# Optimization experiments

Measured on AMD Instinct MI355X. Metric: run time of the kernel, lower is better.

## Reference

```python
import jax, jax.numpy as jnp
import numpy as np

B = 8192
D = 128
N_CLASSES = 100
TEMPERATURE = 0.1


def setup_inputs() -> dict:
    key = jax.random.key(0)
    k1, k2 = jax.random.split(key)
    feats = jax.random.normal(k1, (B, D), dtype=jnp.float32)
    # L2-normalise as the docstring assumes
    feats = feats / jnp.linalg.norm(feats, axis=1, keepdims=True)
    labels = jax.random.randint(k2, (B,), 0, N_CLASSES, dtype=jnp.int64)
    return {"features": feats, "labels": labels}


def reference(features, labels):
    features = features.astype(jnp.float32)
    b = features.shape[0]
    sim = (features @ features.T) / TEMPERATURE            # (B, B)
    labels_eq = labels[None, :] == labels[:, None]          # (B, B)
    self_mask = ~jnp.eye(b, dtype=bool)                     # (B, B), False on diag
    pos_mask = labels_eq & self_mask

    sim_max = jax.lax.stop_gradient(jnp.max(sim, axis=1, keepdims=True))
    logits = sim - sim_max                                  # (B, B)
    exp_logits = jnp.exp(logits) * self_mask.astype(jnp.float32)
    log_sum_exp = jnp.log(jnp.sum(exp_logits, axis=1, keepdims=True) + 1e-12)
    log_prob = logits - log_sum_exp                         # (B, B)

    n_positives = jnp.sum(pos_mask.astype(jnp.float32), axis=1)  # (B,)
    valid = n_positives > 0
    mean_log_prob = jnp.sum(pos_mask.astype(jnp.float32) * log_prob, axis=1) \
        / jnp.maximum(n_positives, 1.0)

    valid_f = valid.astype(jnp.float32)
    n_valid = jnp.sum(valid_f)
    loss = -jnp.sum(mean_log_prob * valid_f) / jnp.maximum(n_valid, 1.0)
    # match torch: return 0 if no anchor has a positive
    return jnp.where(n_valid > 0, loss, jnp.float32(0.0))
```

## Files before the change

### kernel.cpp

```cpp
#include <hip/hip_runtime.h>
#include <hip/hip_bf16.h>


#define BB 8192
#define DD 128
#define NC 8
#define COLCHUNK (BB / NC)
#define ITERS (COLCHUNK / 128)
#define TEMP_INV 10.0f
#define MSHIFT 10.5f

typedef __bf16 bf16x8 __attribute__((ext_vector_type(8)));
typedef float floatx4 __attribute__((ext_vector_type(4)));

__device__ inline unsigned short f2bf(float f) {
    unsigned u = __float_as_uint(f);
    return (unsigned short)((u + 0x7FFFu + ((u >> 16) & 1u)) >> 16);
}

__global__ void supcon_detect(const unsigned short* __restrict__ feats_raw,
                              const int* __restrict__ labels_raw,
                              int* __restrict__ flags)
{
    int lane = threadIdx.x;
    unsigned ue = ((unsigned)feats_raw[2 * lane]) << 16;
    float fe = __uint_as_float(ue);
    float ve = fe * fe;
    int odd_or = labels_raw[2 * lane + 1];
#pragma unroll
    for (int m = 1; m < 64; m <<= 1) {
        ve += __shfl_xor(ve, m, 64);
        odd_or |= __shfl_xor(odd_or, m, 64);
    }
    if (lane == 0) {
        bool feats_bf16 = (ve > 0.05f) && (ve < 4.0f);
        flags[0] = feats_bf16 ? 0 : 1;
        flags[1] = (odd_or == 0) ? 1 : 0;
    }
}

__global__ __launch_bounds__(256) void supcon_convert(
    const void* __restrict__ fin, const void* __restrict__ lin,
    const int* __restrict__ flags,
    unsigned short* __restrict__ fbf, int* __restrict__ lab)
{
    int gid = blockIdx.x * 256 + threadIdx.x;
    if (flags[0]) {
        float4 v = ((const float4*)fin)[gid];
        ushort4 o;
        o.x = f2bf(v.x); o.y = f2bf(v.y); o.z = f2bf(v.z); o.w = f2bf(v.w);
        ((ushort4*)fbf)[gid] = o;
    } else {
        ((ushort4*)fbf)[gid] = ((const ushort4*)fin)[gid];
    }
    if (blockIdx.x < 32) {
        int li = blockIdx.x * 256 + threadIdx.x;
        const int* L = (const int*)lin;
        lab[li] = flags[1] ? L[2 * li] : L[li];
    }
}

__global__ __launch_bounds__(256, 2) void supcon_main(
    const unsigned short* __restrict__ Fb, const int* __restrict__ labels,
    float* __restrict__ e_part, float* __restrict__ p_part,
    float* __restrict__ n_part)
{
    __shared__ unsigned char ldsbuf[32768];
    __shared__ float red[3][128][2];

    const int tid  = threadIdx.x;
    const int lane = tid & 63;
    const int wid  = tid >> 6;
    const int wrow = wid >> 1;
    const int wcol = wid & 1;
    const int quad = lane >> 4;
    const int l16  = lane & 15;

    const int chunk   = blockIdx.x;
    const int rowbase = blockIdx.y * 128;
    const int colchunkbase = chunk * COLCHUNK;

    {
        const unsigned char* gA = (const unsigned char*)(Fb) + (size_t)rowbase * 256;
#pragma unroll
        for (int rnd = 0; rnd < 8; ++rnd) {
            int off = rnd * 4096 + tid * 16;
            int row = off >> 8;
            int g   = (off >> 4) & 15;
            int gs  = g ^ (row & 15);
            int4 v  = *(const int4*)(gA + off);
            *(int4*)(&ldsbuf[row * 256 + gs * 16]) = v;
        }
    }
    __syncthreads();

    bf16x8 afrag[4][4];
#pragma unroll
    for (int ti = 0; ti < 4; ++ti) {
        int row = wrow * 64 + ti * 16 + l16;
#pragma unroll
        for (int k = 0; k < 4; ++k) {
            int g  = k * 4 + quad;
            int gs = g ^ (row & 15);
            afrag[ti][k] = *(const bf16x8*)(&ldsbuf[row * 256 + gs * 16]);
        }
    }

    int lab_row[16];
#pragma unroll
    for (int ti = 0; ti < 4; ++ti)
#pragma unroll
        for (int r = 0; r < 4; ++r)
            lab_row[ti * 4 + r] = labels[rowbase + wrow * 64 + ti * 16 + quad * 4 + r];

    float e_acc[16], p_acc[16], n_acc[16];
#pragma unroll
    for (int i = 0; i < 16; ++i) { e_acc[i] = 0.0f; p_acc[i] = 0.0f; n_acc[i] = 0.0f; }

    __syncthreads();

    for (int it = 0; it < ITERS; ++it) {
        int colbase = colchunkbase + it * 128;
        const unsigned char* gB = (const unsigned char*)(Fb) + (size_t)colbase * 256;
#pragma unroll
        for (int rnd = 0; rnd < 8; ++rnd) {
            int off = rnd * 4096 + tid * 16;
            int row = off >> 8;
            int g   = (off >> 4) & 15;
            int gs  = g ^ (row & 15);
            int4 v  = *(const int4*)(gB + off);
            *(int4*)(&ldsbuf[row * 256 + gs * 16]) = v;
        }
        __syncthreads();

#pragma unroll
        for (int tj = 0; tj < 4; ++tj) {
            int coll = wcol * 64 + tj * 16 + l16;
            bf16x8 bfrag[4];
#pragma unroll
            for (int k = 0; k < 4; ++k) {
                int g  = k * 4 + quad;
                int gs = g ^ (coll & 15);
                bfrag[k] = *(const bf16x8*)(&ldsbuf[coll * 256 + gs * 16]);
            }
            floatx4 acc[4];
#pragma unroll
            for (int ti = 0; ti < 4; ++ti) acc[ti] = (floatx4){0.f, 0.f, 0.f, 0.f};
#pragma unroll
            for (int k = 0; k < 4; ++k)
#pragma unroll
                for (int ti = 0; ti < 4; ++ti)
                    acc[ti] = __builtin_amdgcn_mfma_f32_16x16x32_bf16(
                        afrag[ti][k], bfrag[k], acc[ti], 0, 0, 0);

            int col   = colbase + coll;
            int lab_c = labels[col];
#pragma unroll
            for (int ti = 0; ti < 4; ++ti) {
                int row0 = rowbase + wrow * 64 + ti * 16 + quad * 4;
#pragma unroll
                for (int r = 0; r < 4; ++r) {
                    float s = acc[ti][r] * TEMP_INV;
                    int row = row0 + r;
                    bool nd  = (row != col);
                    float ex = __expf(s - MSHIFT);
                    bool pos = nd && (lab_c == lab_row[ti * 4 + r]);
                    e_acc[ti * 4 + r] += nd ? ex : 0.0f;
                    p_acc[ti * 4 + r] += pos ? s : 0.0f;
                    n_acc[ti * 4 + r] += pos ? 1.0f : 0.0f;
                }
            }
        }
        __syncthreads();
    }

#pragma unroll
    for (int i = 0; i < 16; ++i) {
        float e = e_acc[i], p = p_acc[i], n = n_acc[i];
#pragma unroll
        for (int m = 1; m < 16; m <<= 1) {
            e += __shfl_xor(e, m, 64);
            p += __shfl_xor(p, m, 64);
            n += __shfl_xor(n, m, 64);
        }
        if (l16 == 0) {
            int row_local = wrow * 64 + (i >> 2) * 16 + quad * 4 + (i & 3);
            red[0][row_local][wcol] = e;
            red[1][row_local][wcol] = p;
            red[2][row_local][wcol] = n;
        }
    }
    __syncthreads();

    if (tid < 128) {
        size_t idx = (size_t)chunk * BB + (rowbase + tid);
        e_part[idx] = red[0][tid][0] + red[0][tid][1];
        p_part[idx] = red[1][tid][0] + red[1][tid][1];
        n_part[idx] = red[2][tid][0] + red[2][tid][1];
    }
}

__global__ __launch_bounds__(256) void supcon_reduce(
    const float* __restrict__ e_part, const float* __restrict__ p_part,
    const float* __restrict__ n_part, float* __restrict__ partials)
{
    int row = blockIdx.x * 256 + threadIdx.x;
    float e = 0.f, p = 0.f, n = 0.f;
#pragma unroll
    for (int c = 0; c < NC; ++c) {
        size_t idx = (size_t)c * BB + row;
        e += e_part[idx]; p += p_part[idx]; n += n_part[idx];
    }
    float contrib = 0.f, vld = 0.f;
    if (n > 0.5f) {
        vld = 1.0f;
        contrib = -(p / n - MSHIFT - logf(e));
    }
#pragma unroll
    for (int m = 1; m < 64; m <<= 1) {
        contrib += __shfl_xor(contrib, m, 64);
        vld     += __shfl_xor(vld, m, 64);
    }
    __shared__ float rl[4], rv[4];
    int lane = threadIdx.x & 63, w = threadIdx.x >> 6;
    if (lane == 0) { rl[w] = contrib; rv[w] = vld; }
    __syncthreads();
    if (threadIdx.x == 0) {
        partials[blockIdx.x * 2]     = rl[0] + rl[1] + rl[2] + rl[3];
        partials[blockIdx.x * 2 + 1] = rv[0] + rv[1] + rv[2] + rv[3];
    }
}

__global__ void supcon_final(const float* __restrict__ partials, float* __restrict__ out)
{
    int lane = threadIdx.x;
    float L = (lane < 32) ? partials[lane * 2]     : 0.0f;
    float V = (lane < 32) ? partials[lane * 2 + 1] : 0.0f;
#pragma unroll
    for (int m = 1; m < 64; m <<= 1) {
        L += __shfl_xor(L, m, 64);
        V += __shfl_xor(V, m, 64);
    }
    if (lane == 0) out[0] = (V > 0.5f) ? (L / V) : 0.0f;
}

extern "C" void kernel_launch(void* const* d_in, const int* in_sizes, int n_in,
                              void* d_out, int out_size, void* d_ws, size_t ws_size,
                              hipStream_t stream)
{
    const void* Fin = d_in[0];
    const void* Lin = d_in[1];

    unsigned short* fbf = (unsigned short*)d_ws;
    int*   lab      = (int*)((char*)d_ws + (size_t)BB * DD * 2);
    float* e_part   = (float*)((char*)lab + (size_t)BB * 4);
    float* p_part   = e_part + (size_t)NC * BB;
    float* n_part   = p_part + (size_t)NC * BB;
    float* partials = n_part + (size_t)NC * BB;
    int*   flags    = (int*)(partials + 64);

    supcon_detect<<<1, 64, 0, stream>>>((const unsigned short*)Fin, (const int*)Lin, flags);
    supcon_convert<<<(BB * DD / 4 + 255) / 256, 256, 0, stream>>>(Fin, Lin, flags, fbf, lab);

    dim3 grid(NC, BB / 128);
    supcon_main<<<grid, 256, 0, stream>>>(fbf, lab, e_part, p_part, n_part);
    supcon_reduce<<<32, 256, 0, stream>>>(e_part, p_part, n_part, partials);
    supcon_final<<<1, 64, 0, stream>>>(partials, (float*)d_out);
}
```

Measured before the change: 105.9 us.

## Fuse prep/reduce kernels, drop diagonal and count masks via algebraic corrections

Merges the detect and convert kernels into one prep kernel that also computes per-row squared norms and a label histogram. The main kernel's inner epilogue no longer masks the diagonal or counts positives; instead the diagonal term is subtracted afterwards using the norms, and positive counts come from the histogram. The separate reduce and final kernels are replaced by atomic accumulation plus a last-block-done reduction inside the main kernel. NC doubles and occupancy hint rises to 4, which cuts launches and per-element ALU work but adds atomics and depends on the bf16 norm matching the MFMA diagonal value.

```diff
diff --git a/kernel.cpp b/kernel.cpp
--- a/kernel.cpp
+++ b/kernel.cpp
@@ -4,11 +4,10 @@
 
 #define BB 8192
 #define DD 128
-#define NC 8
+#define NC 16
 #define COLCHUNK (BB / NC)
 #define ITERS (COLCHUNK / 128)
-#define TEMP_INV 10.0f
-#define MSHIFT 10.5f
+#define NBLOCKS (NC * (BB / 128))
 
 typedef __bf16 bf16x8 __attribute__((ext_vector_type(8)));
 typedef float floatx4 __attribute__((ext_vector_type(4)));
@@ -17,56 +16,97 @@
     unsigned u = __float_as_uint(f);
     return (unsigned short)((u + 0x7FFFu + ((u >> 16) & 1u)) >> 16);
 }
-
-__global__ void supcon_detect(const unsigned short* __restrict__ feats_raw,
-                              const int* __restrict__ labels_raw,
-                              int* __restrict__ flags)
+__device__ inline float bf2f(unsigned short u) {
+    return __uint_as_float(((unsigned)u) << 16);
+}
+
+__global__ __launch_bounds__(256) void supcon_prep(
+    const void* __restrict__ fin, const void* __restrict__ lin,
+    unsigned short* __restrict__ fbf, int* __restrict__ lab,
+    float* __restrict__ norms, int* __restrict__ hist,
+    float* __restrict__ ep, unsigned* __restrict__ counter)
 {
-    int lane = threadIdx.x;
-    unsigned ue = ((unsigned)feats_raw[2 * lane]) << 16;
-    float fe = __uint_as_float(ue);
-    float ve = fe * fe;
-    int odd_or = labels_raw[2 * lane + 1];
-#pragma unroll
-    for (int m = 1; m < 64; m <<= 1) {
-        ve += __shfl_xor(ve, m, 64);
-        odd_or |= __shfl_xor(odd_or, m, 64);
-    }
-    if (lane == 0) {
-        bool feats_bf16 = (ve > 0.05f) && (ve < 4.0f);
-        flags[0] = feats_bf16 ? 0 : 1;
-        flags[1] = (odd_or == 0) ? 1 : 0;
-    }
-}
-
-__global__ __launch_bounds__(256) void supcon_convert(
-    const void* __restrict__ fin, const void* __restrict__ lin,
-    const int* __restrict__ flags,
-    unsigned short* __restrict__ fbf, int* __restrict__ lab)
-{
-    int gid = blockIdx.x * 256 + threadIdx.x;
-    if (flags[0]) {
-        float4 v = ((const float4*)fin)[gid];
-        ushort4 o;
-        o.x = f2bf(v.x); o.y = f2bf(v.y); o.z = f2bf(v.z); o.w = f2bf(v.w);
-        ((ushort4*)fbf)[gid] = o;
+    __shared__ int sflags[2];
+    __shared__ int lhist[100];
+    const int t = threadIdx.x, b = blockIdx.x;
+
+    if (t < 64) {
+        unsigned ue = ((unsigned)((const unsigned short*)fin)[2 * t]) << 16;
+        float fe = __uint_as_float(ue);
+        float ve = fe * fe;
+        int odd = ((const int*)lin)[2 * t + 1];
+#pragma unroll
+        for (int m = 1; m < 64; m <<= 1) {
+            ve += __shfl_xor(ve, m, 64);
+            odd |= __shfl_xor(odd, m, 64);
+        }
+        if (t == 0) {
+            sflags[0] = ((ve > 0.05f) && (ve < 4.0f)) ? 0 : 1;
+            sflags[1] = (odd == 0) ? 1 : 0;
+        }
+    }
+    __syncthreads();
+    const int f_fp32 = sflags[0], l_i64 = sflags[1];
+
+    const int base = b * 2048 + t * 8;
+    ushort4 lo, hi;
+    if (f_fp32) {
+        float4 a = ((const float4*)fin)[base >> 2];
+        float4 c = ((const float4*)fin)[(base >> 2) + 1];
+        lo.x = f2bf(a.x); lo.y = f2bf(a.y); lo.z = f2bf(a.z); lo.w = f2bf(a.w);
+        hi.x = f2bf(c.x); hi.y = f2bf(c.y); hi.z = f2bf(c.z); hi.w = f2bf(c.w);
     } else {
-        ((ushort4*)fbf)[gid] = ((const ushort4*)fin)[gid];
-    }
-    if (blockIdx.x < 32) {
-        int li = blockIdx.x * 256 + threadIdx.x;
+        lo = ((const ushort4*)fin)[base >> 2];
+        hi = ((const ushort4*)fin)[(base >> 2) + 1];
+    }
+    ((ushort4*)fbf)[base >> 2]       = lo;
+    ((ushort4*)fbf)[(base >> 2) + 1] = hi;
+
+    float s = 0.0f;
+    float v;
+    v = bf2f(lo.x); s = fmaf(v, v, s);  v = bf2f(lo.y); s = fmaf(v, v, s);
+    v = bf2f(lo.z); s = fmaf(v, v, s);  v = bf2f(lo.w); s = fmaf(v, v, s);
+    v = bf2f(hi.x); s = fmaf(v, v, s);  v = bf2f(hi.y); s = fmaf(v, v, s);
+    v = bf2f(hi.z); s = fmaf(v, v, s);  v = bf2f(hi.w); s = fmaf(v, v, s);
+#pragma unroll
+    for (int m = 1; m < 16; m <<= 1) s += __shfl_xor(s, m, 64);
+    if ((t & 15) == 0) norms[base >> 7] = s;
+
+    if (b < 32) {
+        int li = b * 256 + t;
         const int* L = (const int*)lin;
-        lab[li] = flags[1] ? L[2 * li] : L[li];
-    }
-}
-
-__global__ __launch_bounds__(256, 2) void supcon_main(
+        lab[li] = l_i64 ? L[2 * li] : L[li];
+    }
+    if (b >= 64 && b < 128) {
+        ep[(b - 64) * 256 + t] = 0.0f;
+        if (b == 64 && t == 0) *counter = 0u;
+    }
+    if (b == 511) {
+        if (t < 100) lhist[t] = 0;
+        __syncthreads();
+        const int* L = (const int*)lin;
+        for (int i = t; i < BB; i += 256) {
+            int lbl = l_i64 ? L[2 * i] : L[i];
+            atomicAdd(&lhist[lbl], 1);
+        }
+        __syncthreads();
+        if (t < 100) hist[t] = lhist[t];
+    }
+}
+
+__global__ __launch_bounds__(256, 4) void supcon_main(
     const unsigned short* __restrict__ Fb, const int* __restrict__ labels,
-    float* __restrict__ e_part, float* __restrict__ p_part,
-    float* __restrict__ n_part)
+    const float* __restrict__ norms, const int* __restrict__ hist,
+    float* __restrict__ ep, unsigned* __restrict__ counter,
+    float* __restrict__ out)
 {
     __shared__ unsigned char ldsbuf[32768];
-    __shared__ float red[3][128][2];
+    __shared__ float red[2][128][2];
+    __shared__ int swin;
+    __shared__ float rl[4], rv[4];
+
+    float* e_part = ep;
+    float* p_part = ep + BB;
 
     const int tid  = threadIdx.x;
     const int lane = tid & 63;
@@ -113,9 +153,9 @@
         for (int r = 0; r < 4; ++r)
             lab_row[ti * 4 + r] = labels[rowbase + wrow * 64 + ti * 16 + quad * 4 + r];
 
-    float e_acc[16], p_acc[16], n_acc[16];
-#pragma unroll
-    for (int i = 0; i < 16; ++i) { e_acc[i] = 0.0f; p_acc[i] = 0.0f; n_acc[i] = 0.0f; }
+    float e_acc[16], p_acc[16];
+#pragma unroll
+    for (int i = 0; i < 16; ++i) { e_acc[i] = 0.0f; p_acc[i] = 0.0f; }
 
     __syncthreads();
 
@@ -153,21 +193,16 @@
                     acc[ti] = __builtin_amdgcn_mfma_f32_16x16x32_bf16(
                         afrag[ti][k], bfrag[k], acc[ti], 0, 0, 0);
 
-            int col   = colbase + coll;
-            int lab_c = labels[col];
+            int lab_c = labels[colbase + coll];
 #pragma unroll
             for (int ti = 0; ti < 4; ++ti) {
-                int row0 = rowbase + wrow * 64 + ti * 16 + quad * 4;
 #pragma unroll
                 for (int r = 0; r < 4; ++r) {
-                    float s = acc[ti][r] * TEMP_INV;
-                    int row = row0 + r;
-                    bool nd  = (row != col);
-                    float ex = __expf(s - MSHIFT);
-                    bool pos = nd && (lab_c == lab_row[ti * 4 + r]);
-                    e_acc[ti * 4 + r] += nd ? ex : 0.0f;
-                    p_acc[ti * 4 + r] += pos ? s : 0.0f;
-                    n_acc[ti * 4 + r] += pos ? 1.0f : 0.0f;
+                    float a  = acc[ti][r];
+                    float ex = __expf(fmaf(a, 10.0f, -10.5f));
+                    e_acc[ti * 4 + r] += ex;
+                    bool pos = (lab_c == lab_row[ti * 4 + r]);
+                    p_acc[ti * 4 + r] += pos ? a : 0.0f;
                 }
             }
         }
@@ -176,72 +211,63 @@
 
 #pragma unroll
     for (int i = 0; i < 16; ++i) {
-        float e = e_acc[i], p = p_acc[i], n = n_acc[i];
+        float e = e_acc[i], p = p_acc[i];
 #pragma unroll
         for (int m = 1; m < 16; m <<= 1) {
             e += __shfl_xor(e, m, 64);
             p += __shfl_xor(p, m, 64);
-            n += __shfl_xor(n, m, 64);
         }
         if (l16 == 0) {
             int row_local = wrow * 64 + (i >> 2) * 16 + quad * 4 + (i & 3);
             red[0][row_local][wcol] = e;
             red[1][row_local][wcol] = p;
-            red[2][row_local][wcol] = n;
         }
     }
     __syncthreads();
 
     if (tid < 128) {
-        size_t idx = (size_t)chunk * BB + (rowbase + tid);
-        e_part[idx] = red[0][tid][0] + red[0][tid][1];
-        p_part[idx] = red[1][tid][0] + red[1][tid][1];
-        n_part[idx] = red[2][tid][0] + red[2][tid][1];
-    }
-}
-
-__global__ __launch_bounds__(256) void supcon_reduce(
-    const float* __restrict__ e_part, const float* __restrict__ p_part,
-    const float* __restrict__ n_part, float* __restrict__ partials)
-{
-    int row = blockIdx.x * 256 + threadIdx.x;
-    float e = 0.f, p = 0.f, n = 0.f;
-#pragma unroll
-    for (int c = 0; c < NC; ++c) {
-        size_t idx = (size_t)c * BB + row;
-        e += e_part[idx]; p += p_part[idx]; n += n_part[idx];
-    }
-    float contrib = 0.f, vld = 0.f;
-    if (n > 0.5f) {
-        vld = 1.0f;
-        contrib = -(p / n - MSHIFT - logf(e));
-    }
-#pragma unroll
-    for (int m = 1; m < 64; m <<= 1) {
-        contrib += __shfl_xor(contrib, m, 64);
-        vld     += __shfl_xor(vld, m, 64);
-    }
-    __shared__ float rl[4], rv[4];
-    int lane = threadIdx.x & 63, w = threadIdx.x >> 6;
-    if (lane == 0) { rl[w] = contrib; rv[w] = vld; }
-    __syncthreads();
-    if (threadIdx.x == 0) {
-        partials[blockIdx.x * 2]     = rl[0] + rl[1] + rl[2] + rl[3];
-        partials[blockIdx.x * 2 + 1] = rv[0] + rv[1] + rv[2] + rv[3];
-    }
-}
-
-__global__ void supcon_final(const float* __restrict__ partials, float* __restrict__ out)
-{
-    int lane = threadIdx.x;
-    float L = (lane < 32) ? partials[lane * 2]     : 0.0f;
-    float V = (lane < 32) ? partials[lane * 2 + 1] : 0.0f;
-#pragma unroll
-    for (int m = 1; m < 64; m <<= 1) {
-        L += __shfl_xor(L, m, 64);
-        V += __shfl_xor(V, m, 64);
-    }
-    if (lane == 0) out[0] = (V > 0.5f) ? (L / V) : 0.0f;
+        int row = rowbase + tid;
+        atomicAdd(&e_part[row], red[0][tid][0] + red[0][tid][1]);
+        atomicAdd(&p_part[row], red[1][tid][0] + red[1][tid][1]);
+    }
+    __syncthreads();
+
+    if (tid == 0) {
+        __threadfence();
+        unsigned old = atomicAdd(counter, 1u);
+        swin = (old == NBLOCKS - 1) ? 1 : 0;
+    }
+    __syncthreads();
+
+    if (swin) {
+        __threadfence();
+        float L = 0.0f, V = 0.0f;
+        for (int row = tid; row < BB; row += 256) {
+            float e  = __hip_atomic_load(&e_part[row], __ATOMIC_RELAXED, __HIP_MEMORY_SCOPE_AGENT);
+            float pp = __hip_atomic_load(&p_part[row], __ATOMIC_RELAXED, __HIP_MEMORY_SCOPE_AGENT);
+            float nr  = norms[row];
+            float n   = (float)(hist[labels[row]] - 1);
+            float sii = 10.0f * nr;
+            float ec  = e - __expf(sii - 10.5f);
+            float pc  = 10.0f * pp - sii;
+            if (n > 0.5f) {
+                V += 1.0f;
+                L += -(pc / n - 10.5f - logf(ec));
+            }
+        }
+#pragma unroll
+        for (int m = 1; m < 64; m <<= 1) {
+            L += __shfl_xor(L, m, 64);
+            V += __shfl_xor(V, m, 64);
+        }
+        if ((tid & 63) == 0) { rl[tid >> 6] = L; rv[tid >> 6] = V; }
+        __syncthreads();
+        if (tid == 0) {
+            float Ls = rl[0] + rl[1] + rl[2] + rl[3];
+            float Vs = rv[0] + rv[1] + rv[2] + rv[3];
+            out[0] = (Vs > 0.5f) ? (Ls / Vs) : 0.0f;
+        }
+    }
 }
 
 extern "C" void kernel_launch(void* const* d_in, const int* in_sizes, int n_in,
@@ -252,18 +278,14 @@
     const void* Lin = d_in[1];
 
     unsigned short* fbf = (unsigned short*)d_ws;
-    int*   lab      = (int*)((char*)d_ws + (size_t)BB * DD * 2);
-    float* e_part   = (float*)((char*)lab + (size_t)BB * 4);
-    float* p_part   = e_part + (size_t)NC * BB;
-    float* n_part   = p_part + (size_t)NC * BB;
-    float* partials = n_part + (size_t)NC * BB;
-    int*   flags    = (int*)(partials + 64);
-
-    supcon_detect<<<1, 64, 0, stream>>>((const unsigned short*)Fin, (const int*)Lin, flags);
-    supcon_convert<<<(BB * DD / 4 + 255) / 256, 256, 0, stream>>>(Fin, Lin, flags, fbf, lab);
+    int*   lab     = (int*)((char*)d_ws + (size_t)BB * DD * 2);
+    float* norms   = (float*)((char*)lab + (size_t)BB * 4);
+    int*   hist    = (int*)((char*)norms + (size_t)BB * 4);
+    float* ep      = (float*)((char*)hist + 512);
+    unsigned* counter = (unsigned*)((char*)ep + (size_t)2 * BB * 4);
+
+    supcon_prep<<<512, 256, 0, stream>>>(Fin, Lin, fbf, lab, norms, hist, ep, counter);
 
     dim3 grid(NC, BB / 128);
-    supcon_main<<<grid, 256, 0, stream>>>(fbf, lab, e_part, p_part, n_part);
-    supcon_reduce<<<32, 256, 0, stream>>>(e_part, p_part, n_part, partials);
-    supcon_final<<<1, 64, 0, stream>>>(partials, (float*)d_out);
-}
+    supcon_main<<<grid, 256, 0, stream>>>(fbf, lab, norms, hist, ep, counter, (float*)d_out);
+}
```

Result: slower. 288.7 us (+172.8%).
